# Kernel optimization log

Hardware: AMD Instinct MI355X
Metric: run time of the kernel (lower is better)

Reference implementation:

```python
import jax, jax.numpy as jnp
import numpy as np

V, E, H, A, B, S = 32000, 1024, 1024, 1024, 64, 512

def setup_inputs() -> dict:
    key = jax.random.key(0)
    ks = jax.random.split(key, 20)
    sc = lambda d: 1.0 / np.sqrt(d)
    return {
        "x": jax.random.randint(ks[0], (B,), 0, V),
        "encoder_outputs": jax.random.normal(ks[1], (S, B, H), jnp.float32),
        "h0": jax.random.normal(ks[2], (1, B, H), jnp.float32),
        "c0": jax.random.normal(ks[3], (1, B, H), jnp.float32),
        "Wa": jax.random.normal(ks[4], (A, H), jnp.float32) * sc(H),
        "b_wa": jnp.zeros((A,), jnp.float32),
        "Ua": jax.random.normal(ks[5], (A, H), jnp.float32) * sc(H),
        "b_ua": jnp.zeros((A,), jnp.float32),
        "va": jax.random.normal(ks[6], (1, A), jnp.float32) * sc(A),
        "b_va": jnp.zeros((1,), jnp.float32),
        "emb": jax.random.normal(ks[7], (V, E), jnp.float32) * 0.02,
        "W_ih": jax.random.normal(ks[8], (4 * H, E + H), jnp.float32) * sc(E + H),
        "W_hh": jax.random.normal(ks[9], (4 * H, H), jnp.float32) * sc(H),
        "b_ih": jnp.zeros((4 * H,), jnp.float32),
        "b_hh": jnp.zeros((4 * H,), jnp.float32),
        "W_clf": jax.random.normal(ks[10], (V, H), jnp.float32) * sc(H),
        "b_clf": jnp.zeros((V,), jnp.float32),
    }

def reference(x, encoder_outputs, h0, c0, Wa, b_wa, Ua, b_ua, va, b_va, emb,
              W_ih, W_hh, b_ih, b_hh, W_clf, b_clf):
    # Bahdanau additive attention: scores over time (axis 0)
    tmp1 = jnp.einsum('lbh,ah->lba', h0, Wa) + b_wa            # [1,B,A]
    tmp2 = jnp.einsum('sbh,ah->sba', encoder_outputs, Ua) + b_ua  # [S,B,A]
    scores = jnp.einsum('sba,oa->sbo', jnp.tanh(tmp1 + tmp2), va) + b_va  # [S,B,1]
    w = jax.nn.softmax(scores, axis=0)                          # softmax over S
    ctx = jnp.einsum('sb,sbh->bh', w[..., 0], encoder_outputs)  # [B,H]
    # embed token, concat with context
    inp = jnp.concatenate([emb[x], ctx], axis=-1)               # [B,E+H]
    # single LSTM step (PyTorch gate order i,f,g,o)
    gates = inp @ W_ih.T + b_ih + h0[0] @ W_hh.T + b_hh         # [B,4H]
    i, f, g, o = jnp.split(gates, 4, axis=-1)
    c1 = jax.nn.sigmoid(f) * c0[0] + jax.nn.sigmoid(i) * jnp.tanh(g)
    h1 = jax.nn.sigmoid(o) * jnp.tanh(c1)
    logits = h1 @ W_clf.T + b_clf                               # [B,V]
    return jax.nn.log_softmax(logits, axis=-1)[None]            # [1,B,V]
```

## Files before the change

### kernel.cpp

```cpp
#include <hip/hip_runtime.h>
#include <hip/hip_bf16.h>
#include <math.h>

typedef unsigned short u16;
typedef unsigned int u32;
typedef __attribute__((ext_vector_type(4))) float f32x4;
typedef __attribute__((ext_vector_type(8))) short s16x8;
typedef __attribute__((ext_vector_type(8))) unsigned short u16x8;

#define DEV __device__ __forceinline__


DEV u16 f2bf(float f) {
    union { float f; u32 u; } x{f};
    return (u16)((x.u + 0x7FFFu + ((x.u >> 16) & 1u)) >> 16);
}
DEV float bf2f(u16 h) {
    union { u32 u; float f; } x;
    x.u = ((u32)h) << 16;
    return x.f;
}
DEV float sigm(float x) { return 1.0f / (1.0f + __expf(-x)); }
DEV float tanh_f(float x) {
    float c = fminf(fmaxf(x, -9.0f), 9.0f);
    float e = __expf(2.0f * c);
    return (e - 1.0f) / (e + 1.0f);
}

#define GLL16(g, l) __builtin_amdgcn_global_load_lds( \
    (const __attribute__((address_space(1))) u32*)(g), \
    (__attribute__((address_space(3))) u32*)(l), 16, 0, 0)

__global__ void kzero(float* p, int n) {
    int i = blockIdx.x * blockDim.x + threadIdx.x;
    if (i < n) p[i] = 0.0f;
}

__global__ void kcvt8(const float* __restrict__ in, u16* __restrict__ out, int n8) {
    int i = blockIdx.x * blockDim.x + threadIdx.x;
    if (i >= n8) return;
    float4 f0 = ((const float4*)in)[i * 2];
    float4 f1 = ((const float4*)in)[i * 2 + 1];
    u16x8 o = {f2bf(f0.x), f2bf(f0.y), f2bf(f0.z), f2bf(f0.w),
               f2bf(f1.x), f2bf(f1.y), f2bf(f1.z), f2bf(f1.w)};
    ((u16x8*)out)[i] = o;
}

__global__ __launch_bounds__(256) void kscores(
    const u16* __restrict__ encbf, const u16* __restrict__ Uabf,
    const float* __restrict__ tmp1c, const float* __restrict__ va,
    float* __restrict__ scores)
{
    __shared__ u16 As[128 * 32];
    __shared__ u16 Bs[128 * 32];

    int wg  = blockIdx.x;
    int lin = (wg & 7) * 256 + (wg >> 3);
    int mt  = lin >> 3, nt = lin & 7;

    int t = threadIdx.x;
    int wid = t >> 6, lane = t & 63;
    int wr = wid >> 1, wc = wid & 1;
    int lr = lane & 15, lg = lane >> 4;

    f32x4 acc[4][4];
#pragma unroll
    for (int i = 0; i < 4; i++)
#pragma unroll
        for (int j = 0; j < 4; j++) acc[i][j] = (f32x4){0.f, 0.f, 0.f, 0.f};

    int srow = t >> 2;
    int skel = (t & 3) * 8;
    const u16* ga0 = encbf + (size_t)(mt * 128 + srow) * 1024 + skel;
    const u16* ga1 = ga0 + 64 * 1024;
    const u16* gb0 = Uabf + (size_t)(nt * 128 + srow) * 1024 + skel;
    const u16* gb1 = gb0 + 64 * 1024;
    u16* la0 = &As[t * 8];
    u16* la1 = &As[2048 + t * 8];
    u16* lb0 = &Bs[t * 8];
    u16* lb1 = &Bs[2048 + t * 8];

    const u16* abase = &As[(wr * 64 + lr) * 32 + lg * 8];
    const u16* bbase = &Bs[(wc * 64 + lr) * 32 + lg * 8];

    for (int k0 = 0; k0 < 1024; k0 += 32) {
        __syncthreads();
        GLL16(ga0 + k0, la0);
        GLL16(ga1 + k0, la1);
        GLL16(gb0 + k0, lb0);
        GLL16(gb1 + k0, lb1);
        __syncthreads();

        s16x8 af[4], bfr[4];
#pragma unroll
        for (int i = 0; i < 4; i++) af[i]  = *(const s16x8*)(abase + i * 16 * 32);
#pragma unroll
        for (int j = 0; j < 4; j++) bfr[j] = *(const s16x8*)(bbase + j * 16 * 32);
#pragma unroll
        for (int i = 0; i < 4; i++)
#pragma unroll
            for (int j = 0; j < 4; j++)
                acc[i][j] = __builtin_amdgcn_mfma_f32_16x16x32_bf16(af[i], bfr[j], acc[i][j], 0, 0, 0);
    }

    int colbase = nt * 128 + wc * 64;
    float vaj[4];
#pragma unroll
    for (int j = 0; j < 4; j++) vaj[j] = va[colbase + j * 16 + lr];

#pragma unroll
    for (int i = 0; i < 4; i++) {
        float rs[4] = {0.f, 0.f, 0.f, 0.f};
        int rowloc = wr * 64 + i * 16 + lg * 4;
#pragma unroll
        for (int j = 0; j < 4; j++) {
            int a = colbase + j * 16 + lr;
#pragma unroll
            for (int r = 0; r < 4; r++) {
                int b = (rowloc + r) & 63;
                rs[r] += vaj[j] * tanh_f(acc[i][j][r] + tmp1c[b * 1024 + a]);
            }
        }
#pragma unroll
        for (int m = 1; m < 16; m <<= 1)
#pragma unroll
            for (int r = 0; r < 4; r++) rs[r] += __shfl_xor(rs[r], m, 64);
        if (lr == 0) {
            int mrow = mt * 128 + rowloc;
#pragma unroll
            for (int r = 0; r < 4; r++) atomicAdd(&scores[mrow + r], rs[r]);
        }
    }
}

__global__ __launch_bounds__(256) void kskinny(
    const u16* __restrict__ Abf, int Ktot,
    const float* __restrict__ B1, int K1,
    const float* __restrict__ B2,
    float* __restrict__ Cout, int N, int klen)
{
    __shared__ u16 As[64 * 40];
    __shared__ u16 Bs[128 * 40];

    int nt = blockIdx.x, p = blockIdx.y;
    int t = threadIdx.x;
    int wid = t >> 6, lane = t & 63;
    int lr = lane & 15, lg = lane >> 4;
    int K2 = Ktot - K1;

    f32x4 acc[4][2];
#pragma unroll
    for (int i = 0; i < 4; i++)
#pragma unroll
        for (int j = 0; j < 2; j++) acc[i][j] = (f32x4){0.f, 0.f, 0.f, 0.f};

    int arow = t >> 2, aq = t & 3;
    const u16* ap = Abf + (size_t)arow * Ktot + aq * 8;
    u16* asw = &As[arow * 40 + aq * 8];

    int brow = t >> 1, bhalf = t & 1;
    int n = nt * 128 + brow;
    u16* bsw = &Bs[brow * 40 + bhalf * 16];

    int kbeg = p * klen, kend = kbeg + klen;
    for (int k0 = kbeg; k0 < kend; k0 += 32) {
        __syncthreads();
        *(uint4*)asw = *(const uint4*)(ap + k0);
        int kk = k0 + bhalf * 16;
        const float* bp = (kk < K1) ? (B1 + (size_t)n * K1 + kk)
                                    : (B2 + (size_t)n * K2 + (kk - K1));
        float4 b0 = ((const float4*)bp)[0];
        float4 b1 = ((const float4*)bp)[1];
        float4 b2 = ((const float4*)bp)[2];
        float4 b3 = ((const float4*)bp)[3];
        u16x8 q0 = {f2bf(b0.x), f2bf(b0.y), f2bf(b0.z), f2bf(b0.w),
                    f2bf(b1.x), f2bf(b1.y), f2bf(b1.z), f2bf(b1.w)};
        u16x8 q1 = {f2bf(b2.x), f2bf(b2.y), f2bf(b2.z), f2bf(b2.w),
                    f2bf(b3.x), f2bf(b3.y), f2bf(b3.z), f2bf(b3.w)};
        *(u16x8*)bsw = q0;
        *(u16x8*)(bsw + 8) = q1;
        __syncthreads();

        const u16* abase = &As[lr * 40 + lg * 8];
        const u16* bbase = &Bs[(wid * 32 + lr) * 40 + lg * 8];
        s16x8 af[4], bfr[2];
#pragma unroll
        for (int i = 0; i < 4; i++) af[i]  = *(const s16x8*)(abase + i * 16 * 40);
#pragma unroll
        for (int j = 0; j < 2; j++) bfr[j] = *(const s16x8*)(bbase + j * 16 * 40);
#pragma unroll
        for (int i = 0; i < 4; i++)
#pragma unroll
            for (int j = 0; j < 2; j++)
                acc[i][j] = __builtin_amdgcn_mfma_f32_16x16x32_bf16(af[i], bfr[j], acc[i][j], 0, 0, 0);
    }

#pragma unroll
    for (int i = 0; i < 4; i++)
#pragma unroll
        for (int j = 0; j < 2; j++) {
            int m = i * 16 + lg * 4;
            int col = nt * 128 + wid * 32 + j * 16 + lr;
#pragma unroll
            for (int r = 0; r < 4; r++)
                Cout[((size_t)(p * 64 + m + r)) * N + col] = acc[i][j][r];
        }
}

__global__ void kredbias(const float* __restrict__ part, const float* __restrict__ bias1,
                         const float* __restrict__ bias2, float* __restrict__ out,
                         int N, int P)
{
    int idx = blockIdx.x * blockDim.x + threadIdx.x;
    if (idx >= 64 * N) return;
    int n = idx % N;
    float v = bias1[n] + bias2[n];
    for (int p = 0; p < P; p++) v += part[(size_t)p * 64 * N + idx];
    out[idx] = v;
}

__global__ __launch_bounds__(512) void ksoftmax_w(const float* __restrict__ scores,
                                                  float* __restrict__ w)
{
    int b = blockIdx.x, s = threadIdx.x;
    __shared__ float red[8], red2[8];
    float v = scores[s * 64 + b];
    float m = v;
#pragma unroll
    for (int mask = 1; mask < 64; mask <<= 1) m = fmaxf(m, __shfl_xor(m, mask, 64));
    if ((s & 63) == 0) red[s >> 6] = m;
    __syncthreads();
#pragma unroll
    for (int k = 0; k < 8; k++) m = fmaxf(m, red[k]);
    float e = __expf(v - m);
    float sum = e;
#pragma unroll
    for (int mask = 1; mask < 64; mask <<= 1) sum += __shfl_xor(sum, mask, 64);
    if ((s & 63) == 0) red2[s >> 6] = sum;
    __syncthreads();
    sum = 0.f;
#pragma unroll
    for (int k = 0; k < 8; k++) sum += red2[k];
    w[s * 64 + b] = e / sum;
}

__global__ __launch_bounds__(256) void kctx(const u16* __restrict__ encbf,
                                            const float* __restrict__ w,
                                            float* __restrict__ pctx)
{
    int b = blockIdx.x & 63, ch = blockIdx.x >> 6;
    int h4 = threadIdx.x;
    float4 acc = {0.f, 0.f, 0.f, 0.f};
    int s0 = ch * 64;
#pragma unroll 4
    for (int si = 0; si < 64; si++) {
        int s = s0 + si;
        float wv = w[s * 64 + b];
        ushort4 e = ((const ushort4*)(encbf + ((size_t)(s * 64 + b)) * 1024))[h4];
        acc.x += wv * bf2f(e.x); acc.y += wv * bf2f(e.y);
        acc.z += wv * bf2f(e.z); acc.w += wv * bf2f(e.w);
    }
    ((float4*)pctx)[((size_t)(ch * 64 + b)) * 256 + h4] = acc;
}

__global__ void kbuild(const int* __restrict__ x, const float* __restrict__ emb,
                       const float* __restrict__ pctx, const float* __restrict__ h0,
                       u16* __restrict__ inp2bf)
{
    int idx = blockIdx.x * blockDim.x + threadIdx.x;
    if (idx >= 64 * 3072) return;
    int b = idx / 3072, k = idx % 3072;
    float v;
    if (k < 1024) {
        v = emb[(size_t)x[b] * 1024 + k];
    } else if (k < 2048) {
        int h = k - 1024;
        v = 0.f;
        for (int p = 0; p < 8; p++) v += pctx[(size_t)(p * 64 + b) * 1024 + h];
    } else {
        v = h0[b * 1024 + (k - 2048)];
    }
    inp2bf[idx] = f2bf(v);
}

__global__ void klstm(const float* __restrict__ gp, const float* __restrict__ b_ih,
                      const float* __restrict__ b_hh, const float* __restrict__ c0,
                      u16* __restrict__ h1bf)
{
    int idx = blockIdx.x * blockDim.x + threadIdx.x;
    int b = idx >> 10, j = idx & 1023;
    float ig = b_ih[j] + b_hh[j];
    float fg = b_ih[1024 + j] + b_hh[1024 + j];
    float gg = b_ih[2048 + j] + b_hh[2048 + j];
    float og = b_ih[3072 + j] + b_hh[3072 + j];
    for (int p = 0; p < 8; p++) {
        const float* g = gp + ((size_t)p * 64 + b) * 4096;
        ig += g[j]; fg += g[1024 + j]; gg += g[2048 + j]; og += g[3072 + j];
    }
    float c = sigm(fg) * c0[idx] + sigm(ig) * tanh_f(gg);
    float h = sigm(og) * tanh_f(c);
    h1bf[idx] = f2bf(h);
}

__global__ __launch_bounds__(1024) void klogsoftmax(const float* __restrict__ logits,
                                                    const float* __restrict__ b_clf,
                                                    float* __restrict__ out)
{
    int b = blockIdx.x, t = threadIdx.x;
    __shared__ float red[16], red2[16];
    float v[32];
    float mx = -1e30f;
#pragma unroll
    for (int i = 0; i < 32; i++) {
        int idx = t + i * 1024;
        if (idx < 32000) {
            v[i] = logits[(size_t)b * 32000 + idx] + b_clf[idx];
            mx = fmaxf(mx, v[i]);
        } else v[i] = -1e30f;
    }
#pragma unroll
    for (int mask = 1; mask < 64; mask <<= 1) mx = fmaxf(mx, __shfl_xor(mx, mask, 64));
    if ((t & 63) == 0) red[t >> 6] = mx;
    __syncthreads();
#pragma unroll
    for (int k = 0; k < 16; k++) mx = fmaxf(mx, red[k]);
    float s = 0.f;
#pragma unroll
    for (int i = 0; i < 32; i++) {
        int idx = t + i * 1024;
        if (idx < 32000) s += __expf(v[i] - mx);
    }
#pragma unroll
    for (int mask = 1; mask < 64; mask <<= 1) s += __shfl_xor(s, mask, 64);
    if ((t & 63) == 0) red2[t >> 6] = s;
    __syncthreads();
    s = 0.f;
#pragma unroll
    for (int k = 0; k < 16; k++) s += red2[k];
    float lse = mx + logf(s);
#pragma unroll
    for (int i = 0; i < 32; i++) {
        int idx = t + i * 1024;
        if (idx < 32000) out[(size_t)b * 32000 + idx] = v[i] - lse;
    }
}

extern "C" void kernel_launch(void* const* d_in, const int* in_sizes, int n_in,
                              void* d_out, int out_size, void* d_ws, size_t ws_size,
                              hipStream_t stream)
{
    const int*   x     = (const int*)d_in[0];
    const float* enc   = (const float*)d_in[1];
    const float* h0    = (const float*)d_in[2];
    const float* c0    = (const float*)d_in[3];
    const float* Wa    = (const float*)d_in[4];
    const float* b_wa  = (const float*)d_in[5];
    const float* Ua    = (const float*)d_in[6];
    const float* b_ua  = (const float*)d_in[7];
    const float* va    = (const float*)d_in[8];
    const float* emb   = (const float*)d_in[10];
    const float* W_ih  = (const float*)d_in[11];
    const float* W_hh  = (const float*)d_in[12];
    const float* b_ih  = (const float*)d_in[13];
    const float* b_hh  = (const float*)d_in[14];
    const float* W_clf = (const float*)d_in[15];
    const float* b_clf = (const float*)d_in[16];
    float* out = (float*)d_out;

    char* ws = (char*)d_ws;
    u16*   encbf    = (u16*)  (ws + 0);
    float* gparts   = (float*)(ws + 0);
    float* logits   = (float*)(ws + 8388608);
    float* scores   = (float*)(ws + 67108864);
    float* wbuf     = (float*)(ws + 67239936);
    float* tmp1part = (float*)(ws + 67371008);
    float* tmp1c    = (float*)(ws + 69468160);
    u16*   h0bf     = (u16*)  (ws + 69730304);
    u16*   Uabf     = (u16*)  (ws + 69861376);
    float* pctx     = (float*)(ws + 71958528);
    u16*   inp2bf   = (u16*)  (ws + 74055680);
    u16*   h1bf     = (u16*)  (ws + 74448896);

    kzero<<<128, 256, 0, stream>>>(scores, 32768);
    kcvt8<<<16384, 256, 0, stream>>>(enc, encbf, 33554432 / 8);
    kcvt8<<<512, 256, 0, stream>>>(Ua, Uabf, 1048576 / 8);
    kcvt8<<<32, 256, 0, stream>>>(h0, h0bf, 65536 / 8);

    {
        dim3 g(8, 8);
        kskinny<<<g, 256, 0, stream>>>(h0bf, 1024, Wa, 1024, nullptr, tmp1part, 1024, 128);
    }
    kredbias<<<256, 256, 0, stream>>>(tmp1part, b_wa, b_ua, tmp1c, 1024, 8);

    kscores<<<2048, 256, 0, stream>>>(encbf, Uabf, tmp1c, va, scores);
    ksoftmax_w<<<64, 512, 0, stream>>>(scores, wbuf);
    kctx<<<512, 256, 0, stream>>>(encbf, wbuf, pctx);
    kbuild<<<768, 256, 0, stream>>>(x, emb, pctx, h0, inp2bf);

    {
        dim3 g(32, 8);
        kskinny<<<g, 256, 0, stream>>>(inp2bf, 3072, W_ih, 2048, W_hh, gparts, 4096, 384);
    }
    klstm<<<256, 256, 0, stream>>>(gparts, b_ih, b_hh, c0, h1bf);

    {
        dim3 g(250, 1);
        kskinny<<<g, 256, 0, stream>>>(h1bf, 1024, W_clf, 1024, nullptr, logits, 32000, 1024);
    }
    klogsoftmax<<<64, 1024, 0, stream>>>(logits, b_clf, out);
}
```

Before: 260.6 us.

## Triple-buffer scores GEMM with 256-row tiles and split-K the classifier GEMM

Rewrites the attention-scores GEMM with 256x128 tiles on 512 threads. It uses a three-slot LDS ring with XOR-swizzled layout, async global-to-LDS prefetch two K-steps ahead, and setprio around the MFMA bursts. The aim is to hide load latency and cut LDS bank conflicts, at the cost of one block per CU and large LDS use. Separately, the classifier GEMM is split four ways along K to fill more CUs. The log-softmax then sums the four partial logits, which adds extra global traffic.

```diff
diff --git a/kernel.cpp b/kernel.cpp
--- a/kernel.cpp
+++ b/kernel.cpp
@@ -46,21 +46,20 @@
     ((u16x8*)out)[i] = o;
 }
 
-__global__ __launch_bounds__(256) void kscores(
+__global__ __launch_bounds__(512, 1) void kscores256(
     const u16* __restrict__ encbf, const u16* __restrict__ Uabf,
     const float* __restrict__ tmp1c, const float* __restrict__ va,
     float* __restrict__ scores)
 {
-    __shared__ u16 As[128 * 32];
-    __shared__ u16 Bs[128 * 32];
+    __shared__ u16 lds[73728];
 
     int wg  = blockIdx.x;
-    int lin = (wg & 7) * 256 + (wg >> 3);
+    int lin = (wg & 7) * 128 + (wg >> 3);
     int mt  = lin >> 3, nt = lin & 7;
 
     int t = threadIdx.x;
     int wid = t >> 6, lane = t & 63;
-    int wr = wid >> 1, wc = wid & 1;
+    int wm = wid >> 1, wn = wid & 1;
     int lr = lane & 15, lg = lane >> 4;
 
     f32x4 acc[4][4];
@@ -69,41 +68,80 @@
 #pragma unroll
         for (int j = 0; j < 4; j++) acc[i][j] = (f32x4){0.f, 0.f, 0.f, 0.f};
 
-    int srow = t >> 2;
-    int skel = (t & 3) * 8;
-    const u16* ga0 = encbf + (size_t)(mt * 128 + srow) * 1024 + skel;
-    const u16* ga1 = ga0 + 64 * 1024;
-    const u16* gb0 = Uabf + (size_t)(nt * 128 + srow) * 1024 + skel;
-    const u16* gb1 = gb0 + 64 * 1024;
-    u16* la0 = &As[t * 8];
-    u16* la1 = &As[2048 + t * 8];
-    u16* lb0 = &Bs[t * 8];
-    u16* lb1 = &Bs[2048 + t * 8];
-
-    const u16* abase = &As[(wr * 64 + lr) * 32 + lg * 8];
-    const u16* bbase = &Bs[(wc * 64 + lr) * 32 + lg * 8];
-
-    for (int k0 = 0; k0 < 1024; k0 += 32) {
-        __syncthreads();
-        GLL16(ga0 + k0, la0);
-        GLL16(ga1 + k0, la1);
-        GLL16(gb0 + k0, lb0);
-        GLL16(gb1 + k0, lb1);
-        __syncthreads();
-
-        s16x8 af[4], bfr[4];
-#pragma unroll
-        for (int i = 0; i < 4; i++) af[i]  = *(const s16x8*)(abase + i * 16 * 32);
-#pragma unroll
-        for (int j = 0; j < 4; j++) bfr[j] = *(const s16x8*)(bbase + j * 16 * 32);
+    int r64  = t >> 3;
+    int kcol = ((t & 7) ^ (r64 & 7)) * 8;
+    const u16* asrc = encbf + (size_t)(mt * 256 + r64) * 1024 + kcol;
+    const u16* bsrc = Uabf + (size_t)(nt * 128 + r64) * 1024 + kcol;
+#define STAGE_A(slot, kofs, q) GLL16(asrc + (size_t)(q) * 64 * 1024 + (kofs), \
+    lds + (slot) * 24576 + (q) * 4096 + t * 8)
+#define STAGE_B(slot, kofs, q) GLL16(bsrc + (size_t)(q) * 64 * 1024 + (kofs), \
+    lds + (slot) * 24576 + 16384 + (q) * 4096 + t * 8)
+
+    int xorm = (lr & 7) * 8;
+    int aoff = (wm * 64 + lr) * 64;
+    int boff = 16384 + (wn * 64 + lr) * 64;
+
+    STAGE_A(0, 0, 0); STAGE_A(0, 0, 1); STAGE_A(0, 0, 2); STAGE_A(0, 0, 3);
+    STAGE_B(0, 0, 0); STAGE_B(0, 0, 1);
+    STAGE_A(1, 64, 0); STAGE_A(1, 64, 1); STAGE_A(1, 64, 2); STAGE_A(1, 64, 3);
+    STAGE_B(1, 64, 0); STAGE_B(1, 64, 1);
+    asm volatile("s_waitcnt vmcnt(6)" ::: "memory");
+    __builtin_amdgcn_s_barrier();
+    __builtin_amdgcn_sched_barrier(0);
+
+    int cs = 0, ss = 2;
+    for (int T = 0; T < 16; T++) {
+        int kt = (T + 2 <= 15) ? (T + 2) : 15;
+        int kofs = kt * 64;
+        const u16* Ac = lds + cs * 24576;
+
+        s16x8 af[4], bf[4];
 #pragma unroll
         for (int i = 0; i < 4; i++)
+            af[i] = *(const s16x8*)(Ac + aoff + i * 1024 + ((lg * 8) ^ xorm));
+#pragma unroll
+        for (int j = 0; j < 4; j++)
+            bf[j] = *(const s16x8*)(Ac + boff + j * 1024 + ((lg * 8) ^ xorm));
+        STAGE_A(ss, kofs, 0); STAGE_A(ss, kofs, 1); STAGE_A(ss, kofs, 2);
+        __builtin_amdgcn_s_barrier();
+        asm volatile("s_waitcnt lgkmcnt(0)" ::: "memory");
+        __builtin_amdgcn_sched_barrier(0);
+        __builtin_amdgcn_s_setprio(1);
+#pragma unroll
+        for (int i = 0; i < 4; i++)
 #pragma unroll
             for (int j = 0; j < 4; j++)
-                acc[i][j] = __builtin_amdgcn_mfma_f32_16x16x32_bf16(af[i], bfr[j], acc[i][j], 0, 0, 0);
-    }
-
-    int colbase = nt * 128 + wc * 64;
+                acc[i][j] = __builtin_amdgcn_mfma_f32_16x16x32_bf16(af[i], bf[j], acc[i][j], 0, 0, 0);
+        __builtin_amdgcn_s_setprio(0);
+        __builtin_amdgcn_s_barrier();
+        __builtin_amdgcn_sched_barrier(0);
+
+#pragma unroll
+        for (int i = 0; i < 4; i++)
+            af[i] = *(const s16x8*)(Ac + aoff + i * 1024 + ((32 + lg * 8) ^ xorm));
+#pragma unroll
+        for (int j = 0; j < 4; j++)
+            bf[j] = *(const s16x8*)(Ac + boff + j * 1024 + ((32 + lg * 8) ^ xorm));
+        STAGE_A(ss, kofs, 3); STAGE_B(ss, kofs, 0); STAGE_B(ss, kofs, 1);
+        asm volatile("s_waitcnt vmcnt(6)" ::: "memory");
+        __builtin_amdgcn_s_barrier();
+        asm volatile("s_waitcnt lgkmcnt(0)" ::: "memory");
+        __builtin_amdgcn_sched_barrier(0);
+        __builtin_amdgcn_s_setprio(1);
+#pragma unroll
+        for (int i = 0; i < 4; i++)
+#pragma unroll
+            for (int j = 0; j < 4; j++)
+                acc[i][j] = __builtin_amdgcn_mfma_f32_16x16x32_bf16(af[i], bf[j], acc[i][j], 0, 0, 0);
+        __builtin_amdgcn_s_setprio(0);
+        __builtin_amdgcn_s_barrier();
+        __builtin_amdgcn_sched_barrier(0);
+
+        cs = (cs == 2) ? 0 : cs + 1;
+        ss = (ss == 2) ? 0 : ss + 1;
+    }
+
+    int colbase = nt * 128 + wn * 64;
     float vaj[4];
 #pragma unroll
     for (int j = 0; j < 4; j++) vaj[j] = va[colbase + j * 16 + lr];
@@ -111,7 +149,7 @@
 #pragma unroll
     for (int i = 0; i < 4; i++) {
         float rs[4] = {0.f, 0.f, 0.f, 0.f};
-        int rowloc = wr * 64 + i * 16 + lg * 4;
+        int rowloc = wm * 64 + i * 16 + lg * 4;
 #pragma unroll
         for (int j = 0; j < 4; j++) {
             int a = colbase + j * 16 + lr;
@@ -126,11 +164,14 @@
 #pragma unroll
             for (int r = 0; r < 4; r++) rs[r] += __shfl_xor(rs[r], m, 64);
         if (lr == 0) {
-            int mrow = mt * 128 + rowloc;
+            int mrow = mt * 256 + rowloc;
 #pragma unroll
             for (int r = 0; r < 4; r++) atomicAdd(&scores[mrow + r], rs[r]);
         }
     }
+    asm volatile("s_waitcnt vmcnt(0)" ::: "memory");
+#undef STAGE_A
+#undef STAGE_B
 }
 
 __global__ __launch_bounds__(256) void kskinny(
@@ -302,7 +343,7 @@
     h1bf[idx] = f2bf(h);
 }
 
-__global__ __launch_bounds__(1024) void klogsoftmax(const float* __restrict__ logits,
+__global__ __launch_bounds__(1024) void klogsoftmax(const float* __restrict__ lp,
                                                     const float* __restrict__ b_clf,
                                                     float* __restrict__ out)
 {
@@ -314,7 +355,11 @@
     for (int i = 0; i < 32; i++) {
         int idx = t + i * 1024;
         if (idx < 32000) {
-            v[i] = logits[(size_t)b * 32000 + idx] + b_clf[idx];
+            float s = b_clf[idx];
+#pragma unroll
+            for (int p = 0; p < 4; p++)
+                s += lp[((size_t)(p * 64 + b)) * 32000 + idx];
+            v[i] = s;
             mx = fmaxf(mx, v[i]);
         } else v[i] = -1e30f;
     }
@@ -370,7 +415,7 @@
     char* ws = (char*)d_ws;
     u16*   encbf    = (u16*)  (ws + 0);
     float* gparts   = (float*)(ws + 0);
-    float* logits   = (float*)(ws + 8388608);
+    float* lparts   = (float*)(ws + 8388608);
     float* scores   = (float*)(ws + 67108864);
     float* wbuf     = (float*)(ws + 67239936);
     float* tmp1part = (float*)(ws + 67371008);
@@ -392,7 +437,7 @@
     }
     kredbias<<<256, 256, 0, stream>>>(tmp1part, b_wa, b_ua, tmp1c, 1024, 8);
 
-    kscores<<<2048, 256, 0, stream>>>(encbf, Uabf, tmp1c, va, scores);
+    kscores256<<<1024, 512, 0, stream>>>(encbf, Uabf, tmp1c, va, scores);
     ksoftmax_w<<<64, 512, 0, stream>>>(scores, wbuf);
     kctx<<<512, 256, 0, stream>>>(encbf, wbuf, pctx);
     kbuild<<<768, 256, 0, stream>>>(x, emb, pctx, h0, inp2bf);
@@ -404,8 +449,8 @@
     klstm<<<256, 256, 0, stream>>>(gparts, b_ih, b_hh, c0, h1bf);
 
     {
-        dim3 g(250, 1);
-        kskinny<<<g, 256, 0, stream>>>(h1bf, 1024, W_clf, 1024, nullptr, logits, 32000, 1024);
-    }
-    klogsoftmax<<<64, 1024, 0, stream>>>(logits, b_clf, out);
-}
+        dim3 g(250, 4);
+        kskinny<<<g, 256, 0, stream>>>(h1bf, 1024, W_clf, 1024, nullptr, lparts, 32000, 256);
+    }
+    klogsoftmax<<<64, 1024, 0, stream>>>(lparts, b_clf, out);
+}
```

Result: faster. 251.2 us (-3.6%).

## Widen scores GEMM K-tile with swizzled LDS, stage tmp1 in LDS, split-K classifier

Applied to the files above, without the earlier changes.

The attention-scores GEMM now loads a 64-wide K slice per iteration into an XOR-swizzled LDS layout, halving barrier rounds and avoiding bank conflicts. It also requests two blocks per CU. The epilogue stages the tmp1 bias tile in LDS instead of gathering it from global memory per element. The classifier GEMM is split along K into four partial outputs that the log-softmax kernel sums, giving 1000 blocks instead of 250 for better CU fill, at the cost of extra partial-sum traffic.

```diff
diff --git a/kernel.cpp b/kernel.cpp
--- a/kernel.cpp
+++ b/kernel.cpp
@@ -46,13 +46,12 @@
     ((u16x8*)out)[i] = o;
 }
 
-__global__ __launch_bounds__(256) void kscores(
+__global__ __launch_bounds__(256, 2) void kscores128(
     const u16* __restrict__ encbf, const u16* __restrict__ Uabf,
     const float* __restrict__ tmp1c, const float* __restrict__ va,
     float* __restrict__ scores)
 {
-    __shared__ u16 As[128 * 32];
-    __shared__ u16 Bs[128 * 32];
+    __shared__ __align__(16) u16 shm[16896];
 
     int wg  = blockIdx.x;
     int lin = (wg & 7) * 256 + (wg >> 3);
@@ -69,44 +68,59 @@
 #pragma unroll
         for (int j = 0; j < 4; j++) acc[i][j] = (f32x4){0.f, 0.f, 0.f, 0.f};
 
-    int srow = t >> 2;
-    int skel = (t & 3) * 8;
-    const u16* ga0 = encbf + (size_t)(mt * 128 + srow) * 1024 + skel;
-    const u16* ga1 = ga0 + 64 * 1024;
-    const u16* gb0 = Uabf + (size_t)(nt * 128 + srow) * 1024 + skel;
-    const u16* gb1 = gb0 + 64 * 1024;
-    u16* la0 = &As[t * 8];
-    u16* la1 = &As[2048 + t * 8];
-    u16* lb0 = &Bs[t * 8];
-    u16* lb1 = &Bs[2048 + t * 8];
-
-    const u16* abase = &As[(wr * 64 + lr) * 32 + lg * 8];
-    const u16* bbase = &Bs[(wc * 64 + lr) * 32 + lg * 8];
-
-    for (int k0 = 0; k0 < 1024; k0 += 32) {
+    int srow = t >> 3;
+    int sq   = ((t & 7) ^ (srow & 7)) * 8;
+    const u16* asrc = encbf + (size_t)(mt * 128 + srow) * 1024 + sq;
+    const u16* bsrc = Uabf + (size_t)(nt * 128 + srow) * 1024 + sq;
+    u16* As = shm;
+    u16* Bs = shm + 8192;
+
+    const u16* A0 = &shm[(wr * 64 + lr) * 64];
+    const u16* B0 = &shm[8192 + (wc * 64 + lr) * 64];
+    int o0 = (lg * 8) ^ ((lr & 7) * 8);
+    int o1 = (32 + lg * 8) ^ ((lr & 7) * 8);
+
+    for (int k0 = 0; k0 < 1024; k0 += 64) {
         __syncthreads();
-        GLL16(ga0 + k0, la0);
-        GLL16(ga1 + k0, la1);
-        GLL16(gb0 + k0, lb0);
-        GLL16(gb1 + k0, lb1);
+#pragma unroll
+        for (int r = 0; r < 4; r++) {
+            GLL16(asrc + k0 + (size_t)r * 32 * 1024, As + r * 2048 + t * 8);
+            GLL16(bsrc + k0 + (size_t)r * 32 * 1024, Bs + r * 2048 + t * 8);
+        }
         __syncthreads();
 
-        s16x8 af[4], bfr[4];
-#pragma unroll
-        for (int i = 0; i < 4; i++) af[i]  = *(const s16x8*)(abase + i * 16 * 32);
-#pragma unroll
-        for (int j = 0; j < 4; j++) bfr[j] = *(const s16x8*)(bbase + j * 16 * 32);
+        s16x8 af[4], bf[4];
+#pragma unroll
+        for (int i = 0; i < 4; i++) af[i] = *(const s16x8*)(A0 + i * 1024 + o0);
+#pragma unroll
+        for (int j = 0; j < 4; j++) bf[j] = *(const s16x8*)(B0 + j * 1024 + o0);
 #pragma unroll
         for (int i = 0; i < 4; i++)
 #pragma unroll
             for (int j = 0; j < 4; j++)
-                acc[i][j] = __builtin_amdgcn_mfma_f32_16x16x32_bf16(af[i], bfr[j], acc[i][j], 0, 0, 0);
-    }
-
-    int colbase = nt * 128 + wc * 64;
+                acc[i][j] = __builtin_amdgcn_mfma_f32_16x16x32_bf16(af[i], bf[j], acc[i][j], 0, 0, 0);
+#pragma unroll
+        for (int i = 0; i < 4; i++) af[i] = *(const s16x8*)(A0 + i * 1024 + o1);
+#pragma unroll
+        for (int j = 0; j < 4; j++) bf[j] = *(const s16x8*)(B0 + j * 1024 + o1);
+#pragma unroll
+        for (int i = 0; i < 4; i++)
+#pragma unroll
+            for (int j = 0; j < 4; j++)
+                acc[i][j] = __builtin_amdgcn_mfma_f32_16x16x32_bf16(af[i], bf[j], acc[i][j], 0, 0, 0);
+    }
+
+    __syncthreads();
+    float* ltmp = (float*)shm;
+    for (int i2 = t; i2 < 8192; i2 += 256) {
+        int b = i2 >> 7, a = i2 & 127;
+        ltmp[b * 132 + a] = tmp1c[b * 1024 + nt * 128 + a];
+    }
+    __syncthreads();
+
     float vaj[4];
 #pragma unroll
-    for (int j = 0; j < 4; j++) vaj[j] = va[colbase + j * 16 + lr];
+    for (int j = 0; j < 4; j++) vaj[j] = va[nt * 128 + wc * 64 + j * 16 + lr];
 
 #pragma unroll
     for (int i = 0; i < 4; i++) {
@@ -114,11 +128,11 @@
         int rowloc = wr * 64 + i * 16 + lg * 4;
 #pragma unroll
         for (int j = 0; j < 4; j++) {
-            int a = colbase + j * 16 + lr;
+            int al = wc * 64 + j * 16 + lr;
 #pragma unroll
             for (int r = 0; r < 4; r++) {
                 int b = (rowloc + r) & 63;
-                rs[r] += vaj[j] * tanh_f(acc[i][j][r] + tmp1c[b * 1024 + a]);
+                rs[r] += vaj[j] * tanh_f(acc[i][j][r] + ltmp[b * 132 + al]);
             }
         }
 #pragma unroll
@@ -302,7 +316,7 @@
     h1bf[idx] = f2bf(h);
 }
 
-__global__ __launch_bounds__(1024) void klogsoftmax(const float* __restrict__ logits,
+__global__ __launch_bounds__(1024) void klogsoftmax(const float* __restrict__ lp,
                                                     const float* __restrict__ b_clf,
                                                     float* __restrict__ out)
 {
@@ -314,7 +328,11 @@
     for (int i = 0; i < 32; i++) {
         int idx = t + i * 1024;
         if (idx < 32000) {
-            v[i] = logits[(size_t)b * 32000 + idx] + b_clf[idx];
+            float s = b_clf[idx];
+#pragma unroll
+            for (int p = 0; p < 4; p++)
+                s += lp[((size_t)(p * 64 + b)) * 32000 + idx];
+            v[i] = s;
             mx = fmaxf(mx, v[i]);
         } else v[i] = -1e30f;
     }
@@ -370,7 +388,7 @@
     char* ws = (char*)d_ws;
     u16*   encbf    = (u16*)  (ws + 0);
     float* gparts   = (float*)(ws + 0);
-    float* logits   = (float*)(ws + 8388608);
+    float* lparts   = (float*)(ws + 8388608);
     float* scores   = (float*)(ws + 67108864);
     float* wbuf     = (float*)(ws + 67239936);
     float* tmp1part = (float*)(ws + 67371008);
@@ -392,7 +410,7 @@
     }
     kredbias<<<256, 256, 0, stream>>>(tmp1part, b_wa, b_ua, tmp1c, 1024, 8);
 
-    kscores<<<2048, 256, 0, stream>>>(encbf, Uabf, tmp1c, va, scores);
+    kscores128<<<2048, 256, 0, stream>>>(encbf, Uabf, tmp1c, va, scores);
     ksoftmax_w<<<64, 512, 0, stream>>>(scores, wbuf);
     kctx<<<512, 256, 0, stream>>>(encbf, wbuf, pctx);
     kbuild<<<768, 256, 0, stream>>>(x, emb, pctx, h0, inp2bf);
@@ -404,8 +422,8 @@
     klstm<<<256, 256, 0, stream>>>(gparts, b_ih, b_hh, c0, h1bf);
 
     {
-        dim3 g(250, 1);
-        kskinny<<<g, 256, 0, stream>>>(h1bf, 1024, W_clf, 1024, nullptr, logits, 32000, 1024);
-    }
-    klogsoftmax<<<64, 1024, 0, stream>>>(logits, b_clf, out);
-}
+        dim3 g(250, 4);
+        kskinny<<<g, 256, 0, stream>>>(h1bf, 1024, W_clf, 1024, nullptr, lparts, 32000, 256);
+    }
+    klogsoftmax<<<64, 1024, 0, stream>>>(lparts, b_clf, out);
+}
```

After: 240.8 us. -7.6%, faster.
